# Optimization experiments

Hardware: AMD Instinct MI355X
Metric: run time of the kernel (lower is better)

Reference implementation:

```python
import jax, jax.numpy as jnp
import numpy as np

N, E = 40000, 640000
DIN, C, EDIM = 128, 128, 32  # heads=1, out_channels=128

def setup_inputs() -> dict:
    key = jax.random.key(0)
    ks = jax.random.split(key, 9)
    x = jax.random.normal(ks[0], (N, DIN), dtype=jnp.float32)
    edge_index = jax.random.randint(ks[1], (2, E), 0, N, dtype=jnp.int64)
    edge_attr = jax.random.normal(ks[2], (E, EDIM), dtype=jnp.float32)
    s = 1.0 / np.sqrt(DIN)
    W = jax.random.normal(ks[3], (DIN, C), dtype=jnp.float32) * s
    W_edge = jax.random.normal(ks[4], (EDIM, C), dtype=jnp.float32) / np.sqrt(EDIM)
    att_src = jax.random.normal(ks[5], (C,), dtype=jnp.float32) * s
    att_dst = jax.random.normal(ks[6], (C,), dtype=jnp.float32) * s
    att_edge = jax.random.normal(ks[7], (C,), dtype=jnp.float32) * s
    bias = jnp.zeros((C,), dtype=jnp.float32)
    return {"x": x, "edge_index": edge_index, "edge_attr": edge_attr,
            "W": W, "W_edge": W_edge, "att_src": att_src, "att_dst": att_dst,
            "att_edge": att_edge, "bias": bias}

def reference(x, edge_index, edge_attr, W, W_edge, att_src, att_dst, att_edge, bias):
    # GATConv (heads=1) with edge features
    h = x @ W                      # [N, C] transformed node features
    a_src = h @ att_src            # [N] per-node source attention logits
    a_dst = h @ att_dst            # [N]
    src, dst = edge_index[0], edge_index[1]
    e = edge_attr @ W_edge         # [E, C]
    a_edge = e @ att_edge          # [E]
    alpha = a_src[src] + a_dst[dst] + a_edge            # [E]
    alpha = jax.nn.leaky_relu(alpha, negative_slope=0.2)
    # segment softmax over incoming edges of each destination node
    amax = jax.ops.segment_max(alpha, dst, num_segments=N)
    amax = jnp.where(jnp.isfinite(amax), amax, 0.0)     # empty segments -> -inf guard
    ex = jnp.exp(alpha - amax[dst])
    denom = jax.ops.segment_sum(ex, dst, num_segments=N)
    w = ex / (denom[dst] + 1e-16)                       # PyG softmax epsilon
    out = jax.ops.segment_sum(h[src] * w[:, None], dst, num_segments=N)  # [N, C]
    return out + bias
```

## Files before the change

kernel.cpp:

```cpp
#include <hip/hip_runtime.h>
#include <hip/hip_bf16.h>
#include <hip/hip_fp16.h>


#define DIN 128
#define CCH 128
#define EDIM 32
#define LDK 40

typedef __attribute__((ext_vector_type(8))) short short8v;
typedef __attribute__((ext_vector_type(4))) float f32x4;

__device__ __forceinline__ unsigned short f2b(float v) {
    __hip_bfloat16 b = __float2bfloat16(v);
    return *(unsigned short*)&b;
}
__device__ __forceinline__ float b2f(unsigned short u) {
    return __uint_as_float((unsigned)u << 16);
}
__device__ __forceinline__ unsigned pack_bf2(float a, float b) {
    return (unsigned)f2b(a) | ((unsigned)f2b(b) << 16);
}

__global__ __launch_bounds__(256, 4) void gemm_h(
    const float* __restrict__ x, const float* __restrict__ W,
    const float* __restrict__ att_src, const float* __restrict__ att_dst,
    const float* __restrict__ W_edge, const float* __restrict__ att_edge,
    const int* __restrict__ ei, const float* __restrict__ ea,
    unsigned* __restrict__ hb, float* __restrict__ a_src,
    float* __restrict__ a_dst, unsigned* __restrict__ erec,
    int* __restrict__ count, int N, int E) {
    __shared__ unsigned short xs_h[64 * LDK];
    __shared__ unsigned short xs_l[64 * LDK];
    __shared__ unsigned short wt_h[128 * LDK];
    __shared__ unsigned short wt_l[128 * LDK];
    __shared__ float vpart[8][EDIM];
    __shared__ float vl[EDIM];

    const int t = threadIdx.x;
    const int ln = t & 63;
    const int wv = t >> 6;
    const int lr = ln & 15;
    const int lk = ln >> 4;
    const int row0 = blockIdx.x * 64;

    {
        const int* eid = ei + E;
        const int stride = gridDim.x * 256;
        for (int e = blockIdx.x * 256 + t; e < E; e += stride) {
            int r = atomicAdd(&count[eid[e]], 1);
            ((unsigned short*)&erec[e])[0] = (unsigned short)r;
        }
    }

    {
        int j = t & 31, seg = t >> 5;
        const float* wr = W_edge + j * CCH + seg * 16;
        const float* ar = att_edge + seg * 16;
        float p = 0.0f;
#pragma unroll
        for (int k = 0; k < 16; ++k) p += wr[k] * ar[k];
        vpart[seg][j] = p;
    }
    __syncthreads();
    if (t < EDIM) {
        float s = 0.0f;
#pragma unroll
        for (int i = 0; i < 8; ++i) s += vpart[i][t];
        vl[t] = s;
    }

    f32x4 acc[8];
#pragma unroll
    for (int cf = 0; cf < 8; ++cf) acc[cf] = (f32x4)(0.0f);

    const float4* x4 = (const float4*)x;
    const float4* W4 = (const float4*)W;

    for (int q = 0; q < 4; ++q) {
        __syncthreads();
#pragma unroll
        for (int i = 0; i < 2; ++i) {
            int j4 = t + 256 * i;
            int r = j4 >> 3;
            int f4 = j4 & 7;
            float4 v = x4[(size_t)(row0 + r) * 32 + q * 8 + f4];
            float vv[4] = {v.x, v.y, v.z, v.w};
            unsigned short h[4], l[4];
#pragma unroll
            for (int m = 0; m < 4; ++m) {
                h[m] = f2b(vv[m]);
                l[m] = f2b(vv[m] - b2f(h[m]));
            }
            uint2 uh = make_uint2((unsigned)h[0] | ((unsigned)h[1] << 16),
                                  (unsigned)h[2] | ((unsigned)h[3] << 16));
            uint2 ul = make_uint2((unsigned)l[0] | ((unsigned)l[1] << 16),
                                  (unsigned)l[2] | ((unsigned)l[3] << 16));
            *(uint2*)&xs_h[r * LDK + f4 * 4] = uh;
            *(uint2*)&xs_l[r * LDK + f4 * 4] = ul;
        }
        {
            int kt = t >> 5;
            int ct = t & 31;
            float w4[4][4];
#pragma unroll
            for (int i = 0; i < 4; ++i) {
                float4 v = W4[(size_t)(q * 32 + kt * 4 + i) * 32 + ct];
                w4[i][0] = v.x; w4[i][1] = v.y; w4[i][2] = v.z; w4[i][3] = v.w;
            }
#pragma unroll
            for (int cc = 0; cc < 4; ++cc) {
                unsigned short h[4], l[4];
#pragma unroll
                for (int i = 0; i < 4; ++i) {
                    h[i] = f2b(w4[i][cc]);
                    l[i] = f2b(w4[i][cc] - b2f(h[i]));
                }
                uint2 uh = make_uint2((unsigned)h[0] | ((unsigned)h[1] << 16),
                                      (unsigned)h[2] | ((unsigned)h[3] << 16));
                uint2 ul = make_uint2((unsigned)l[0] | ((unsigned)l[1] << 16),
                                      (unsigned)l[2] | ((unsigned)l[3] << 16));
                int c = ct * 4 + cc;
                *(uint2*)&wt_h[c * LDK + kt * 4] = uh;
                *(uint2*)&wt_l[c * LDK + kt * 4] = ul;
            }
        }
        __syncthreads();

        short8v bh = *(const short8v*)&xs_h[(wv * 16 + lr) * LDK + lk * 8];
        short8v bl = *(const short8v*)&xs_l[(wv * 16 + lr) * LDK + lk * 8];
#pragma unroll
        for (int cf = 0; cf < 8; ++cf) {
            short8v ah = *(const short8v*)&wt_h[(cf * 16 + lr) * LDK + lk * 8];
            short8v al = *(const short8v*)&wt_l[(cf * 16 + lr) * LDK + lk * 8];
            acc[cf] = __builtin_amdgcn_mfma_f32_16x16x32_bf16(ah, bh, acc[cf], 0, 0, 0);
            acc[cf] = __builtin_amdgcn_mfma_f32_16x16x32_bf16(ah, bl, acc[cf], 0, 0, 0);
            acc[cf] = __builtin_amdgcn_mfma_f32_16x16x32_bf16(al, bh, acc[cf], 0, 0, 0);
        }
    }

    {
        const int row = row0 + wv * 16 + lr;
        float ps = 0.0f, pd = 0.0f;
#pragma unroll
        for (int cf = 0; cf < 8; ++cf) {
            int c0 = cf * 16 + lk * 4;
            float4 as4 = *(const float4*)&att_src[c0];
            float4 ad4 = *(const float4*)&att_dst[c0];
            ps += acc[cf][0] * as4.x + acc[cf][1] * as4.y +
                  acc[cf][2] * as4.z + acc[cf][3] * as4.w;
            pd += acc[cf][0] * ad4.x + acc[cf][1] * ad4.y +
                  acc[cf][2] * ad4.z + acc[cf][3] * ad4.w;
            uint2 u = make_uint2(pack_bf2(acc[cf][0], acc[cf][1]),
                                 pack_bf2(acc[cf][2], acc[cf][3]));
            *(uint2*)&hb[(size_t)row * 64 + cf * 8 + lk * 2] = u;
        }
        ps += __shfl_xor(ps, 16);
        ps += __shfl_xor(ps, 32);
        pd += __shfl_xor(pd, 16);
        pd += __shfl_xor(pd, 32);
        if (ln < 16) {
            a_src[row0 + wv * 16 + ln] = ps;
            a_dst[row0 + wv * 16 + ln] = pd;
        }
    }

    {
        float vlr[EDIM];
#pragma unroll
        for (int j = 0; j < EDIM; ++j) vlr[j] = vl[j];
        const float4* ea4 = (const float4*)ea;
        const int e0 = blockIdx.x * 1024 + t;
#pragma unroll
        for (int i = 0; i < 4; ++i) {
            int e = e0 + 256 * i;
            if (e < E) {
                float s = 0.0f;
#pragma unroll
                for (int j = 0; j < 8; ++j) {
                    float4 v = ea4[(size_t)e * 8 + j];
                    s += v.x * vlr[4 * j] + v.y * vlr[4 * j + 1] +
                         v.z * vlr[4 * j + 2] + v.w * vlr[4 * j + 3];
                }
                ((unsigned short*)&erec[e])[1] =
                    __half_as_ushort(__float2half(s));
            }
        }
    }
}

__global__ __launch_bounds__(256) void scan_part(const int* __restrict__ count,
                                                 int* __restrict__ bsum, int N4) {
    int i4 = blockIdx.x * 256 + threadIdx.x;
    int s = 0;
    if (i4 < N4) {
        int4 vv = ((const int4*)count)[i4];
        s = vv.x + vv.y + vv.z + vv.w;
    }
#pragma unroll
    for (int off = 32; off; off >>= 1) s += __shfl_down(s, off);
    __shared__ int wsum[4];
    if ((threadIdx.x & 63) == 0) wsum[threadIdx.x >> 6] = s;
    __syncthreads();
    if (threadIdx.x == 0)
        bsum[blockIdx.x] = wsum[0] + wsum[1] + wsum[2] + wsum[3];
}

__global__ __launch_bounds__(256) void scan_apply(
    const int* __restrict__ count, const int* __restrict__ bsum,
    const float* __restrict__ a_dst, int* __restrict__ offs,
    float2* __restrict__ dinfo, int N4) {
    __shared__ int s_boff;
    __shared__ int wt[4];
    if (threadIdx.x == 0) {
        int s = 0;
        for (int i = 0; i < (int)blockIdx.x; ++i) s += bsum[i];
        s_boff = s;
    }
    int i4 = blockIdx.x * 256 + threadIdx.x;
    int4 vv = make_int4(0, 0, 0, 0);
    if (i4 < N4) vv = ((const int4*)count)[i4];
    int s = vv.x + vv.y + vv.z + vv.w;
    int lane = threadIdx.x & 63, w = threadIdx.x >> 6;
    int inc = s;
#pragma unroll
    for (int off = 1; off < 64; off <<= 1) {
        int u = __shfl_up(inc, off);
        if (lane >= off) inc += u;
    }
    if (lane == 63) wt[w] = inc;
    __syncthreads();
    int woff = 0;
    for (int i = 0; i < w; ++i) woff += wt[i];
    int exd = s_boff + woff + inc - s;
    if (i4 < N4) {
        int4 o;
        o.x = exd;
        o.y = exd + vv.x;
        o.z = exd + vv.x + vv.y;
        o.w = exd + vv.x + vv.y + vv.z;
        ((int4*)offs)[i4] = o;
        float4 ad = ((const float4*)a_dst)[i4];
        float4 d0 = make_float4(ad.x, __int_as_float(o.x),
                                ad.y, __int_as_float(o.y));
        float4 d1 = make_float4(ad.z, __int_as_float(o.z),
                                ad.w, __int_as_float(o.w));
        ((float4*)dinfo)[i4 * 2] = d0;
        ((float4*)dinfo)[i4 * 2 + 1] = d1;
    }
}

__global__ __launch_bounds__(256) void edge_fill(
    const int* __restrict__ ei, const unsigned* __restrict__ erec,
    const float* __restrict__ a_src, const float2* __restrict__ dinfo,
    unsigned* __restrict__ pairs, int E) {
    const int t = threadIdx.x;
    const int base = blockIdx.x * 1024 + t;
    int eidx[4], sn[4], dn[4], rk[4];
    float ae[4];
    bool ok[4];
#pragma unroll
    for (int i = 0; i < 4; ++i) {
        eidx[i] = base + 256 * i;
        ok[i] = eidx[i] < E;
    }
#pragma unroll
    for (int i = 0; i < 4; ++i) {
        sn[i] = ok[i] ? ei[eidx[i]] : 0;
        dn[i] = ok[i] ? ei[E + eidx[i]] : 0;
    }
#pragma unroll
    for (int i = 0; i < 4; ++i) {
        unsigned er = ok[i] ? erec[eidx[i]] : 0u;
        rk[i] = (int)(er & 0xffffu);
        ae[i] = __half2float(__ushort_as_half((unsigned short)(er >> 16)));
    }
    float asv[4];
    float2 di[4];
#pragma unroll
    for (int i = 0; i < 4; ++i) {
        asv[i] = a_src[sn[i]];
        di[i] = dinfo[dn[i]];
    }
#pragma unroll
    for (int i = 0; i < 4; ++i) {
        if (!ok[i]) continue;
        float alpha = asv[i] + di[i].x + ae[i];
        alpha = alpha > 0.0f ? alpha : 0.2f * alpha;
        float ex = __expf(alpha);
        unsigned rec = (unsigned)(unsigned short)sn[i] |
                       ((unsigned)__half_as_ushort(__float2half(ex)) << 16);
        int p = __float_as_int(di[i].y) + rk[i];
        pairs[p] = rec;
    }
}

#define GATHER_EDGE(rec)                                                      \
    {                                                                         \
        unsigned q = hb[(size_t)((rec) & 0xffffu) * 64 + lane];               \
        float exv = __half2float(__ushort_as_half((unsigned short)((rec) >> 16))); \
        a0 += exv * __uint_as_float(q << 16);                                 \
        a1 += exv * __uint_as_float(q & 0xffff0000u);                         \
        sum += exv;                                                           \
    }

__global__ __launch_bounds__(256) void gather_k(
    const int* __restrict__ count, const int* __restrict__ offs,
    const unsigned* __restrict__ pairs, const unsigned* __restrict__ hb,
    const float* __restrict__ bias, float* __restrict__ out, int N) {
    int n = blockIdx.x * 4 + (threadIdx.x >> 6);
    int lane = threadIdx.x & 63;
    if (n >= N) return;
    int cnt = count[n];
    int start = offs[n];
    float a0 = 0.0f, a1 = 0.0f, sum = 0.0f;
    int j = 0;
    int head = (4 - (start & 3)) & 3;
    if (head > cnt) head = cnt;
    for (; j < head; ++j) {
        unsigned r = pairs[start + j];
        GATHER_EDGE(r);
    }
    int nq = (cnt - j) >> 2;
    if (nq > 0) {
        const uint4* pp4 = (const uint4*)(pairs + start + j);
        uint4 cur = pp4[0];
        for (int g = 0; g + 1 < nq; ++g) {
            uint4 nxt = pp4[g + 1];
            unsigned q0 = hb[(size_t)(cur.x & 0xffffu) * 64 + lane];
            unsigned q1 = hb[(size_t)(cur.y & 0xffffu) * 64 + lane];
            unsigned q2 = hb[(size_t)(cur.z & 0xffffu) * 64 + lane];
            unsigned q3 = hb[(size_t)(cur.w & 0xffffu) * 64 + lane];
            float e0 = __half2float(__ushort_as_half((unsigned short)(cur.x >> 16)));
            float e1 = __half2float(__ushort_as_half((unsigned short)(cur.y >> 16)));
            float e2 = __half2float(__ushort_as_half((unsigned short)(cur.z >> 16)));
            float e3 = __half2float(__ushort_as_half((unsigned short)(cur.w >> 16)));
            a0 += e0 * __uint_as_float(q0 << 16);
            a1 += e0 * __uint_as_float(q0 & 0xffff0000u);
            a0 += e1 * __uint_as_float(q1 << 16);
            a1 += e1 * __uint_as_float(q1 & 0xffff0000u);
            a0 += e2 * __uint_as_float(q2 << 16);
            a1 += e2 * __uint_as_float(q2 & 0xffff0000u);
            a0 += e3 * __uint_as_float(q3 << 16);
            a1 += e3 * __uint_as_float(q3 & 0xffff0000u);
            sum += (e0 + e1) + (e2 + e3);
            cur = nxt;
        }
        {
            unsigned q0 = hb[(size_t)(cur.x & 0xffffu) * 64 + lane];
            unsigned q1 = hb[(size_t)(cur.y & 0xffffu) * 64 + lane];
            unsigned q2 = hb[(size_t)(cur.z & 0xffffu) * 64 + lane];
            unsigned q3 = hb[(size_t)(cur.w & 0xffffu) * 64 + lane];
            float e0 = __half2float(__ushort_as_half((unsigned short)(cur.x >> 16)));
            float e1 = __half2float(__ushort_as_half((unsigned short)(cur.y >> 16)));
            float e2 = __half2float(__ushort_as_half((unsigned short)(cur.z >> 16)));
            float e3 = __half2float(__ushort_as_half((unsigned short)(cur.w >> 16)));
            a0 += e0 * __uint_as_float(q0 << 16);
            a1 += e0 * __uint_as_float(q0 & 0xffff0000u);
            a0 += e1 * __uint_as_float(q1 << 16);
            a1 += e1 * __uint_as_float(q1 & 0xffff0000u);
            a0 += e2 * __uint_as_float(q2 << 16);
            a1 += e2 * __uint_as_float(q2 & 0xffff0000u);
            a0 += e3 * __uint_as_float(q3 << 16);
            a1 += e3 * __uint_as_float(q3 & 0xffff0000u);
            sum += (e0 + e1) + (e2 + e3);
        }
        j += nq * 4;
    }
    for (; j < cnt; ++j) {
        unsigned r = pairs[start + j];
        GATHER_EDGE(r);
    }
    float inv = 1.0f / (sum + 1e-16f);
    float2 bv = *(const float2*)&bias[2 * lane];
    float2 o;
    o.x = a0 * inv + bv.x;
    o.y = a1 * inv + bv.y;
    *(float2*)&out[(size_t)n * CCH + 2 * lane] = o;
}

extern "C" void kernel_launch(void* const* d_in, const int* in_sizes, int n_in,
                              void* d_out, int out_size, void* d_ws, size_t ws_size,
                              hipStream_t stream) {
    const float* x        = (const float*)d_in[0];
    const int*   ei       = (const int*)d_in[1];
    const float* ea       = (const float*)d_in[2];
    const float* W        = (const float*)d_in[3];
    const float* W_edge   = (const float*)d_in[4];
    const float* att_src  = (const float*)d_in[5];
    const float* att_dst  = (const float*)d_in[6];
    const float* att_edge = (const float*)d_in[7];
    const float* bias     = (const float*)d_in[8];
    float* out = (float*)d_out;

    const int N = in_sizes[0] / DIN;
    const int E = in_sizes[2] / EDIM;
    const int N4 = N / 4;
    const int NB = (N4 + 255) / 256;

    char* ws = (char*)d_ws;
    unsigned* hb    = (unsigned*)ws;
    unsigned* pairs = (unsigned*)(ws + (size_t)N * 64 * 4);
    unsigned* erec  = pairs + E;
    float*  a_src = (float*)(erec + E);
    float*  a_dst = a_src + N;
    float2* dinfo = (float2*)(a_dst + N);
    int*    count = (int*)(dinfo + N);
    int*    offs  = count + N;
    int*    bsum  = offs + N;

    hipMemsetAsync(count, 0, (size_t)N * sizeof(int), stream);

    gemm_h<<<N / 64, 256, 0, stream>>>(x, W, att_src, att_dst, W_edge, att_edge,
                                       ei, ea, hb, a_src, a_dst, erec,
                                       count, N, E);
    scan_part<<<NB, 256, 0, stream>>>(count, bsum, N4);
    scan_apply<<<NB, 256, 0, stream>>>(count, bsum, a_dst, offs, dinfo, N4);
    edge_fill<<<(E + 1023) / 1024, 256, 0, stream>>>(ei, erec, a_src, dinfo,
                                                     pairs, E);
    gather_k<<<(N + 3) / 4, 256, 0, stream>>>(count, offs, pairs, hb, bias, out, N);
}
```

Measured before the change: 238.9 us.

## Split gemm grid into GEMM and edge blocks, pad counters, single-block scan

The fused first kernel now launches three blocks per 64-row tile. One block does the node GEMM and attention logits, and two blocks handle edge work: the destination-count atomics and the edge-attention dot product, written into erec as a single packed store. Per-node counters are padded to 16-byte stride to reduce atomic contention on shared cache lines. The two-kernel scan is replaced by one 1024-thread block scanning 40 entries per thread, and a_dst is written directly into dinfo. This removes a launch and the partial writes, at the cost of a serial single-block scan and a larger zeroed counter buffer.

```diff
diff --git a/kernel.cpp b/kernel.cpp
--- a/kernel.cpp
+++ b/kernel.cpp
@@ -28,8 +28,8 @@
     const float* __restrict__ W_edge, const float* __restrict__ att_edge,
     const int* __restrict__ ei, const float* __restrict__ ea,
     unsigned* __restrict__ hb, float* __restrict__ a_src,
-    float* __restrict__ a_dst, unsigned* __restrict__ erec,
-    int* __restrict__ count, int N, int E) {
+    float2* __restrict__ dinfo, unsigned* __restrict__ erec,
+    int* __restrict__ count_p, int N, int E) {
     __shared__ unsigned short xs_h[64 * LDK];
     __shared__ unsigned short xs_l[64 * LDK];
     __shared__ unsigned short wt_h[128 * LDK];
@@ -38,37 +38,62 @@
     __shared__ float vl[EDIM];
 
     const int t = threadIdx.x;
+    const int g = blockIdx.x / 3;
+    const int r = blockIdx.x % 3;
+
+    if (r != 0) {
+        {
+            int j = t & 31, seg = t >> 5;
+            const float* wr = W_edge + j * CCH + seg * 16;
+            const float* ar = att_edge + seg * 16;
+            float p = 0.0f;
+#pragma unroll
+            for (int k = 0; k < 16; ++k) p += wr[k] * ar[k];
+            vpart[seg][j] = p;
+        }
+        __syncthreads();
+        if (t < EDIM) {
+            float s = 0.0f;
+#pragma unroll
+            for (int i = 0; i < 8; ++i) s += vpart[i][t];
+            vl[t] = s;
+        }
+        __syncthreads();
+        float vlr[EDIM];
+#pragma unroll
+        for (int j = 0; j < EDIM; ++j) vlr[j] = vl[j];
+
+        const int* eid = ei + E;
+        const float4* ea4 = (const float4*)ea;
+        const int sIdx = g * 2 + (r - 1);
+        const int e0 = sIdx * 512 + t;
+#pragma unroll
+        for (int i = 0; i < 2; ++i) {
+            int e = e0 + 256 * i;
+            if (e < E) {
+                float4 q[8];
+#pragma unroll
+                for (int j = 0; j < 8; ++j) q[j] = ea4[(size_t)e * 8 + j];
+                int dn = eid[e];
+                int rk = atomicAdd(&count_p[dn * 4], 1);
+                float s = 0.0f;
+#pragma unroll
+                for (int j = 0; j < 8; ++j) {
+                    s += q[j].x * vlr[4 * j] + q[j].y * vlr[4 * j + 1] +
+                         q[j].z * vlr[4 * j + 2] + q[j].w * vlr[4 * j + 3];
+                }
+                erec[e] = (unsigned)(unsigned short)rk |
+                          ((unsigned)__half_as_ushort(__float2half(s)) << 16);
+            }
+        }
+        return;
+    }
+
     const int ln = t & 63;
     const int wv = t >> 6;
     const int lr = ln & 15;
     const int lk = ln >> 4;
-    const int row0 = blockIdx.x * 64;
-
-    {
-        const int* eid = ei + E;
-        const int stride = gridDim.x * 256;
-        for (int e = blockIdx.x * 256 + t; e < E; e += stride) {
-            int r = atomicAdd(&count[eid[e]], 1);
-            ((unsigned short*)&erec[e])[0] = (unsigned short)r;
-        }
-    }
-
-    {
-        int j = t & 31, seg = t >> 5;
-        const float* wr = W_edge + j * CCH + seg * 16;
-        const float* ar = att_edge + seg * 16;
-        float p = 0.0f;
-#pragma unroll
-        for (int k = 0; k < 16; ++k) p += wr[k] * ar[k];
-        vpart[seg][j] = p;
-    }
-    __syncthreads();
-    if (t < EDIM) {
-        float s = 0.0f;
-#pragma unroll
-        for (int i = 0; i < 8; ++i) s += vpart[i][t];
-        vl[t] = s;
-    }
+    const int row0 = g * 64;
 
     f32x4 acc[8];
 #pragma unroll
@@ -82,9 +107,9 @@
 #pragma unroll
         for (int i = 0; i < 2; ++i) {
             int j4 = t + 256 * i;
-            int r = j4 >> 3;
+            int rr = j4 >> 3;
             int f4 = j4 & 7;
-            float4 v = x4[(size_t)(row0 + r) * 32 + q * 8 + f4];
+            float4 v = x4[(size_t)(row0 + rr) * 32 + q * 8 + f4];
             float vv[4] = {v.x, v.y, v.z, v.w};
             unsigned short h[4], l[4];
 #pragma unroll
@@ -96,8 +121,8 @@
                                   (unsigned)h[2] | ((unsigned)h[3] << 16));
             uint2 ul = make_uint2((unsigned)l[0] | ((unsigned)l[1] << 16),
                                   (unsigned)l[2] | ((unsigned)l[3] << 16));
-            *(uint2*)&xs_h[r * LDK + f4 * 4] = uh;
-            *(uint2*)&xs_l[r * LDK + f4 * 4] = ul;
+            *(uint2*)&xs_h[rr * LDK + f4 * 4] = uh;
+            *(uint2*)&xs_l[rr * LDK + f4 * 4] = ul;
         }
         {
             int kt = t >> 5;
@@ -160,93 +185,47 @@
         pd += __shfl_xor(pd, 16);
         pd += __shfl_xor(pd, 32);
         if (ln < 16) {
-            a_src[row0 + wv * 16 + ln] = ps;
-            a_dst[row0 + wv * 16 + ln] = pd;
-        }
-    }
-
-    {
-        float vlr[EDIM];
-#pragma unroll
-        for (int j = 0; j < EDIM; ++j) vlr[j] = vl[j];
-        const float4* ea4 = (const float4*)ea;
-        const int e0 = blockIdx.x * 1024 + t;
-#pragma unroll
-        for (int i = 0; i < 4; ++i) {
-            int e = e0 + 256 * i;
-            if (e < E) {
-                float s = 0.0f;
-#pragma unroll
-                for (int j = 0; j < 8; ++j) {
-                    float4 v = ea4[(size_t)e * 8 + j];
-                    s += v.x * vlr[4 * j] + v.y * vlr[4 * j + 1] +
-                         v.z * vlr[4 * j + 2] + v.w * vlr[4 * j + 3];
-                }
-                ((unsigned short*)&erec[e])[1] =
-                    __half_as_ushort(__float2half(s));
-            }
-        }
-    }
-}
-
-__global__ __launch_bounds__(256) void scan_part(const int* __restrict__ count,
-                                                 int* __restrict__ bsum, int N4) {
-    int i4 = blockIdx.x * 256 + threadIdx.x;
+            int rw = row0 + wv * 16 + ln;
+            a_src[rw] = ps;
+            ((float*)&dinfo[rw])[0] = pd;
+        }
+    }
+}
+
+__global__ __launch_bounds__(1024) void scan_one(
+    const int* __restrict__ count_p, int* __restrict__ offs,
+    float2* __restrict__ dinfo, int N) {
+    const int t = threadIdx.x;
+    const int base = t * 40;
+    int c[40];
     int s = 0;
-    if (i4 < N4) {
-        int4 vv = ((const int4*)count)[i4];
-        s = vv.x + vv.y + vv.z + vv.w;
-    }
-#pragma unroll
-    for (int off = 32; off; off >>= 1) s += __shfl_down(s, off);
-    __shared__ int wsum[4];
-    if ((threadIdx.x & 63) == 0) wsum[threadIdx.x >> 6] = s;
-    __syncthreads();
-    if (threadIdx.x == 0)
-        bsum[blockIdx.x] = wsum[0] + wsum[1] + wsum[2] + wsum[3];
-}
-
-__global__ __launch_bounds__(256) void scan_apply(
-    const int* __restrict__ count, const int* __restrict__ bsum,
-    const float* __restrict__ a_dst, int* __restrict__ offs,
-    float2* __restrict__ dinfo, int N4) {
-    __shared__ int s_boff;
-    __shared__ int wt[4];
-    if (threadIdx.x == 0) {
-        int s = 0;
-        for (int i = 0; i < (int)blockIdx.x; ++i) s += bsum[i];
-        s_boff = s;
-    }
-    int i4 = blockIdx.x * 256 + threadIdx.x;
-    int4 vv = make_int4(0, 0, 0, 0);
-    if (i4 < N4) vv = ((const int4*)count)[i4];
-    int s = vv.x + vv.y + vv.z + vv.w;
-    int lane = threadIdx.x & 63, w = threadIdx.x >> 6;
+#pragma unroll
+    for (int i = 0; i < 40; ++i) {
+        int n = base + i;
+        c[i] = (n < N) ? count_p[n * 4] : 0;
+        s += c[i];
+    }
+    int lane = t & 63, w = t >> 6;
     int inc = s;
 #pragma unroll
     for (int off = 1; off < 64; off <<= 1) {
         int u = __shfl_up(inc, off);
         if (lane >= off) inc += u;
     }
+    __shared__ int wt[16];
     if (lane == 63) wt[w] = inc;
     __syncthreads();
     int woff = 0;
     for (int i = 0; i < w; ++i) woff += wt[i];
-    int exd = s_boff + woff + inc - s;
-    if (i4 < N4) {
-        int4 o;
-        o.x = exd;
-        o.y = exd + vv.x;
-        o.z = exd + vv.x + vv.y;
-        o.w = exd + vv.x + vv.y + vv.z;
-        ((int4*)offs)[i4] = o;
-        float4 ad = ((const float4*)a_dst)[i4];
-        float4 d0 = make_float4(ad.x, __int_as_float(o.x),
-                                ad.y, __int_as_float(o.y));
-        float4 d1 = make_float4(ad.z, __int_as_float(o.z),
-                                ad.w, __int_as_float(o.w));
-        ((float4*)dinfo)[i4 * 2] = d0;
-        ((float4*)dinfo)[i4 * 2 + 1] = d1;
+    int run = woff + inc - s;
+#pragma unroll
+    for (int i = 0; i < 40; ++i) {
+        int n = base + i;
+        if (n < N) {
+            offs[n] = run;
+            ((int*)&dinfo[n])[1] = run;
+            run += c[i];
+        }
     }
 }
 
@@ -305,13 +284,13 @@
     }
 
 __global__ __launch_bounds__(256) void gather_k(
-    const int* __restrict__ count, const int* __restrict__ offs,
+    const int* __restrict__ count_p, const int* __restrict__ offs,
     const unsigned* __restrict__ pairs, const unsigned* __restrict__ hb,
     const float* __restrict__ bias, float* __restrict__ out, int N) {
     int n = blockIdx.x * 4 + (threadIdx.x >> 6);
     int lane = threadIdx.x & 63;
     if (n >= N) return;
-    int cnt = count[n];
+    int cnt = count_p[n * 4];
     int start = offs[n];
     float a0 = 0.0f, a1 = 0.0f, sum = 0.0f;
     int j = 0;
@@ -395,28 +374,23 @@
 
     const int N = in_sizes[0] / DIN;
     const int E = in_sizes[2] / EDIM;
-    const int N4 = N / 4;
-    const int NB = (N4 + 255) / 256;
 
     char* ws = (char*)d_ws;
     unsigned* hb    = (unsigned*)ws;
     unsigned* pairs = (unsigned*)(ws + (size_t)N * 64 * 4);
     unsigned* erec  = pairs + E;
-    float*  a_src = (float*)(erec + E);
-    float*  a_dst = a_src + N;
-    float2* dinfo = (float2*)(a_dst + N);
-    int*    count = (int*)(dinfo + N);
-    int*    offs  = count + N;
-    int*    bsum  = offs + N;
-
-    hipMemsetAsync(count, 0, (size_t)N * sizeof(int), stream);
-
-    gemm_h<<<N / 64, 256, 0, stream>>>(x, W, att_src, att_dst, W_edge, att_edge,
-                                       ei, ea, hb, a_src, a_dst, erec,
-                                       count, N, E);
-    scan_part<<<NB, 256, 0, stream>>>(count, bsum, N4);
-    scan_apply<<<NB, 256, 0, stream>>>(count, bsum, a_dst, offs, dinfo, N4);
+    float2* dinfo   = (float2*)(erec + E);
+    int*    count_p = (int*)(dinfo + N);
+    int*    offs    = count_p + N * 4;
+    float*  a_src   = (float*)(offs + N);
+
+    hipMemsetAsync(count_p, 0, (size_t)N * 16, stream);
+
+    gemm_h<<<3 * (N / 64), 256, 0, stream>>>(x, W, att_src, att_dst, W_edge,
+                                             att_edge, ei, ea, hb, a_src,
+                                             dinfo, erec, count_p, N, E);
+    scan_one<<<1, 1024, 0, stream>>>(count_p, offs, dinfo, N);
     edge_fill<<<(E + 1023) / 1024, 256, 0, stream>>>(ei, erec, a_src, dinfo,
                                                      pairs, E);
-    gather_k<<<(N + 3) / 4, 256, 0, stream>>>(count, offs, pairs, hb, bias, out, N);
-}
+    gather_k<<<(N + 3) / 4, 256, 0, stream>>>(count_p, offs, pairs, hb, bias, out, N);
+}
```

After: 284.6 us. 1.19x slower.
